# Kernel tuning notes

Hardware: AMD Instinct MI355X
Metric: run time of the kernel (lower is better)

## Reference

```python
import jax, jax.numpy as jnp
import numpy as np

L_RTN = 3  # complex taps produced by the RTN head (w_rtn3 out dim = 2*L_RTN)
EPS = 1e-12


def _to_complex(x):
    # (B, 2n) real interleaved [re0, im0, re1, im1, ...] -> (B, n) complex
    return x[:, 0::2] + 1j * x[:, 1::2]


def _to_real(xc):
    # (B, n) complex -> (B, 2n) real interleaved
    b, n = xc.shape
    return jnp.stack([xc.real, xc.imag], axis=-1).reshape(b, 2 * n)


def _complex_conv_taps(h_c, x_c):
    # per-sample causal complex FIR: out[t] = sum_l h[l] * x[t-l]
    # h_c: (B, L) complex, x_c: (B, n) complex
    n = x_c.shape[1]
    out = jnp.zeros_like(x_c)
    for l in range(h_c.shape[1]):  # L is tiny and static
        shifted = jnp.pad(x_c, ((0, 0), (l, 0)))[:, :n]
        out = out + h_c[:, l:l + 1] * shifted
    return out


def setup_inputs() -> dict:
    key = jax.random.key(0)
    ks = jax.random.split(key, 16)
    B, D_IN, H1, CH, H_RTN, H2, D_OUT = 8192, 512, 4096, 256, 1024, 4096, 512
    s = 0.02  # weight init scale
    x = jax.random.normal(ks[0], (B, D_IN), jnp.float32)
    w1 = s * jax.random.normal(ks[1], (H1, D_IN), jnp.float32)
    b1 = jnp.zeros((H1,), jnp.float32)
    w2 = s * jax.random.normal(ks[2], (CH, H1), jnp.float32)
    b2 = jnp.zeros((CH,), jnp.float32)
    w_rtn1 = s * jax.random.normal(ks[3], (H_RTN, CH), jnp.float32)
    b_rtn1 = jnp.zeros((H_RTN,), jnp.float32)
    w_rtn2 = s * jax.random.normal(ks[4], (H_RTN, H_RTN), jnp.float32)
    b_rtn2 = jnp.zeros((H_RTN,), jnp.float32)
    w_rtn3 = s * jax.random.normal(ks[5], (2 * L_RTN, H_RTN), jnp.float32)
    # bias so that RTN starts near identity tap [1, 0, 0, ...]
    b_rtn3 = jnp.zeros((2 * L_RTN,), jnp.float32).at[0].set(1.0)
    w3 = s * jax.random.normal(ks[6], (H2, CH), jnp.float32)
    b3 = jnp.zeros((H2,), jnp.float32)
    w4 = s * jax.random.normal(ks[7], (D_OUT, H2), jnp.float32)
    b4 = jnp.zeros((D_OUT,), jnp.float32)
    h = jax.random.normal(ks[8], (2,), jnp.float32)
    h = h / jnp.linalg.norm(h)  # unit-power single-tap fading channel
    noise = 0.1 * jax.random.normal(ks[9], (B, CH), jnp.float32)
    return {"x": x, "w1": w1, "b1": b1, "w2": w2, "b2": b2,
            "w_rtn1": w_rtn1, "b_rtn1": b_rtn1, "w_rtn2": w_rtn2,
            "b_rtn2": b_rtn2, "w_rtn3": w_rtn3, "b_rtn3": b_rtn3,
            "w3": w3, "b3": b3, "w4": w4, "b4": b4, "h": h, "noise": noise}


def reference(x, w1, b1, w2, b2, w_rtn1, b_rtn1, w_rtn2, b_rtn2,
              w_rtn3, b_rtn3, w3, b3, w4, b4, h, noise):
    # encoder (linear1 -> relu -> linear2)
    a = jax.nn.relu(x @ w1.T + b1)
    s = a @ w2.T + b2                      # (B, 2n) channel signal
    # power normalization: sqrt(2n) * sqrt(0.5) * s / ||s||
    scale = jnp.sqrt(s.shape[1] * 0.5)
    s = scale * s / jnp.linalg.norm(s, axis=1, keepdims=True)
    tx_c = _to_complex(s)                  # (B, n) transmitted symbols
    # single-tap complex channel
    h_c = h[0] + 1j * h[1]
    y = _to_real(h_c * tx_c) + noise       # add per-sample AWGN
    y_c = _to_complex(y)
    # LS channel estimate (1 tap): h_est = <y, x> / <x, x>
    num = jnp.sum(y_c * jnp.conj(tx_c), axis=1, keepdims=True)
    den = jnp.sum(jnp.abs(tx_c) ** 2, axis=1, keepdims=True)
    h_est = num / den                      # (B, 1)
    # zero-forcing signal estimate
    x_eq = y_c * jnp.conj(h_est) / (jnp.abs(h_est) ** 2 + EPS)
    xr = _to_real(x_eq)                    # (B, 2n)
    # RTN: predict inverse taps and apply per-sample complex conv
    g = jnp.tanh(xr @ w_rtn1.T + b_rtn1)
    g = jnp.tanh(g @ w_rtn2.T + b_rtn2)
    h_inv = g @ w_rtn3.T + b_rtn3          # (B, 2*L_RTN)
    h_inv_c = h_inv[:, 0::2] + 1j * h_inv[:, 1::2]
    xr = _to_real(_complex_conv_taps(h_inv_c, _to_complex(xr)))
    # decoder (linear3 -> relu -> linear4)
    out = jax.nn.relu(xr @ w3.T + b3)
    return out @ w4.T + b4
```

## Files before the change

### kernel.cpp

```cpp
#include <hip/hip_runtime.h>
#include <hip/hip_bf16.h>
#include <math.h>

using bf16 = __hip_bfloat16;
typedef __attribute__((ext_vector_type(8))) short short8;
typedef __attribute__((ext_vector_type(4))) float float4v;

template <typename T> __device__ inline T cvt_out(float v);
template <> __device__ inline float cvt_out<float>(float v) { return v; }
template <> __device__ inline bf16 cvt_out<bf16>(float v) { return __float2bfloat16(v); }

__device__ inline void gload_lds16(const bf16* g, bf16* l) {
    __builtin_amdgcn_global_load_lds(
        (const __attribute__((address_space(1))) void*)g,
        (__attribute__((address_space(3))) void*)l, 16, 0, 0);
}

struct CvtPack {
    const float* src[7];
    bf16* dst[7];
    int end[7];
};

__global__ __launch_bounds__(256) void cvt_all(CvtPack p) {
    int e = (blockIdx.x * 256 + threadIdx.x) * 4;
    int start = 0;
#pragma unroll
    for (int s = 0; s < 7; ++s) {
        if (e < p.end[s]) {
            int off = e - start;
            float4 v = *(const float4*)(p.src[s] + off);
            bf16* d = p.dst[s] + off;
            d[0] = __float2bfloat16(v.x);
            d[1] = __float2bfloat16(v.y);
            d[2] = __float2bfloat16(v.z);
            d[3] = __float2bfloat16(v.w);
            return;
        }
        start = p.end[s];
    }
}

__global__ __launch_bounds__(256) void reduce2_bias(const float* __restrict__ p0,
                                                    const float* __restrict__ p1,
                                                    const float* __restrict__ bias,
                                                    float* __restrict__ out,
                                                    int nmask, int total4) {
    int i = blockIdx.x * 256 + threadIdx.x;
    if (i < total4) {
        int idx = i * 4;
        float4 a = *(const float4*)(p0 + idx);
        float4 b = *(const float4*)(p1 + idx);
        float4 bb = *(const float4*)(bias + (idx & nmask));
        float4 r;
        r.x = a.x + b.x + bb.x;
        r.y = a.y + b.y + bb.y;
        r.z = a.z + b.z + bb.z;
        r.w = a.w + b.w + bb.w;
        *(float4*)(out + idx) = r;
    }
}

template <int ACT, typename OutT, int WMT, int WNT, int BKT, bool PARTIAL>
__global__ __launch_bounds__(256) void gemm_bt(const bf16* __restrict__ A,
                                               const bf16* __restrict__ W,
                                               const float* __restrict__ bias,
                                               OutT* __restrict__ C,
                                               int M, int N, int K,
                                               int nbn, int kcount) {
    constexpr int TBM = 32 * WMT;
    constexpr int TBN = 32 * WNT;
    constexpr int CPR = BKT / 8;
    constexpr int CA = TBM * CPR;
    constexpr int CB = TBN * CPR;

    __shared__ bf16 As[TBM * BKT];
    __shared__ bf16 Bs[TBN * BKT];

    const int bi = blockIdx.x;
    const int xcd = bi & 7, t = bi >> 3;
    const int bn = t % nbn;
    const int bm = xcd + 8 * (t / nbn);
    const int kbeg = PARTIAL ? blockIdx.y * kcount : 0;
    OutT* Cp = PARTIAL ? C + (size_t)blockIdx.y * M * N : C;

    const int tid = threadIdx.x;
    const int wave = tid >> 6, lane = tid & 63;
    const int wm = (wave >> 1) * (16 * WMT), wn = (wave & 1) * (16 * WNT);
    const int quad = lane >> 4, lrow = lane & 15;

    float4v acc[WMT][WNT] = {};
    const size_t arow = (size_t)(bm * TBM) * K;
    const size_t brow = (size_t)(bn * TBN) * K;

    for (int k0 = kbeg; k0 < kbeg + kcount; k0 += BKT) {
        __syncthreads();
#pragma unroll
        for (int tt = 0; tt < CA / 256; ++tt) {
            int base = tt * 256 + wave * 64;
            int c = base + lane;
            int row = c / CPR, col = (c % CPR) * 8;
            gload_lds16(A + arow + (size_t)row * K + k0 + col, As + base * 8);
        }
#pragma unroll
        for (int tt = 0; tt < CB / 256; ++tt) {
            int base = tt * 256 + wave * 64;
            int c = base + lane;
            int row = c / CPR, col = (c % CPR) * 8;
            gload_lds16(W + brow + (size_t)row * K + k0 + col, Bs + base * 8);
        }
        __syncthreads();
#pragma unroll
        for (int kk = 0; kk < BKT; kk += 32) {
            short8 af[WMT], bfr[WNT];
#pragma unroll
            for (int i = 0; i < WMT; ++i)
                af[i] = *(const short8*)(As + (wm + i * 16 + lrow) * BKT + kk + quad * 8);
#pragma unroll
            for (int j = 0; j < WNT; ++j)
                bfr[j] = *(const short8*)(Bs + (wn + j * 16 + lrow) * BKT + kk + quad * 8);
#pragma unroll
            for (int i = 0; i < WMT; ++i)
#pragma unroll
                for (int j = 0; j < WNT; ++j)
                    acc[i][j] = __builtin_amdgcn_mfma_f32_16x16x32_bf16(af[i], bfr[j], acc[i][j], 0, 0, 0);
        }
    }

#pragma unroll
    for (int i = 0; i < WMT; ++i) {
        int m0 = bm * TBM + wm + i * 16 + quad * 4;
#pragma unroll
        for (int j = 0; j < WNT; ++j) {
            int n = bn * TBN + wn + j * 16 + lrow;
            if constexpr (PARTIAL) {
#pragma unroll
                for (int r = 0; r < 4; ++r)
                    Cp[(size_t)(m0 + r) * N + n] = acc[i][j][r];
            } else {
                float bv = bias[n];
#pragma unroll
                for (int r = 0; r < 4; ++r) {
                    float v = acc[i][j][r] + bv;
                    if (ACT == 1) v = fmaxf(v, 0.f);
                    else if (ACT == 2) v = tanhf(v);
                    Cp[(size_t)(m0 + r) * N + n] = cvt_out<OutT>(v);
                }
            }
        }
    }
}

__global__ __launch_bounds__(64) void channel_kernel(const float* __restrict__ s,
                                                     const float* __restrict__ h,
                                                     const float* __restrict__ noise,
                                                     float* __restrict__ xr_f,
                                                     bf16* __restrict__ xr_b) {
    const int b = blockIdx.x, lane = threadIdx.x;
    const float* srow = s + (size_t)b * 256;

    float ss = 0.f;
#pragma unroll
    for (int t = 0; t < 4; ++t) {
        float v = srow[lane + 64 * t];
        ss += v * v;
    }
#pragma unroll
    for (int off = 32; off; off >>= 1) ss += __shfl_xor(ss, off);
    const float inv = sqrtf(128.0f) / sqrtf(ss);

    const float hre = h[0], him = h[1];

    float yre[2], yim[2];
    float nre = 0.f, nim = 0.f, den = 0.f;
#pragma unroll
    for (int t = 0; t < 2; ++t) {
        int c = lane + 64 * t;
        float tr = srow[2 * c] * inv, ti = srow[2 * c + 1] * inv;
        float yr = hre * tr - him * ti + noise[(size_t)b * 256 + 2 * c];
        float yi = hre * ti + him * tr + noise[(size_t)b * 256 + 2 * c + 1];
        yre[t] = yr; yim[t] = yi;
        nre += yr * tr + yi * ti;
        nim += yi * tr - yr * ti;
        den += tr * tr + ti * ti;
    }
#pragma unroll
    for (int off = 32; off; off >>= 1) {
        nre += __shfl_xor(nre, off);
        nim += __shfl_xor(nim, off);
        den += __shfl_xor(den, off);
    }
    const float her = nre / den, hei = nim / den;
    const float d2 = her * her + hei * hei + 1e-12f;

#pragma unroll
    for (int t = 0; t < 2; ++t) {
        int c = lane + 64 * t;
        float xre = (yre[t] * her + yim[t] * hei) / d2;
        float xim = (yim[t] * her - yre[t] * hei) / d2;
        xr_f[(size_t)b * 256 + 2 * c] = xre;
        xr_f[(size_t)b * 256 + 2 * c + 1] = xim;
        xr_b[(size_t)b * 256 + 2 * c] = __float2bfloat16(xre);
        xr_b[(size_t)b * 256 + 2 * c + 1] = __float2bfloat16(xim);
    }
}

__global__ __launch_bounds__(64) void rtn_taps_conv(const bf16* __restrict__ g2,
                                                    const float* __restrict__ wr3,
                                                    const float* __restrict__ br3,
                                                    const float* __restrict__ xr_f,
                                                    bf16* __restrict__ xr2) {
    const int b = blockIdx.x, lane = threadIdx.x;
    const bf16* grow = g2 + (size_t)b * 1024;

    float acc[6] = {0.f, 0.f, 0.f, 0.f, 0.f, 0.f};
#pragma unroll
    for (int t = 0; t < 16; ++t) {
        int k = lane + 64 * t;
        float gv = __bfloat162float(grow[k]);
#pragma unroll
        for (int j = 0; j < 6; ++j) acc[j] += gv * wr3[j * 1024 + k];
    }
#pragma unroll
    for (int j = 0; j < 6; ++j)
#pragma unroll
        for (int off = 32; off; off >>= 1) acc[j] += __shfl_xor(acc[j], off);

    float tre[3], tim[3];
#pragma unroll
    for (int l = 0; l < 3; ++l) {
        tre[l] = acc[2 * l] + br3[2 * l];
        tim[l] = acc[2 * l + 1] + br3[2 * l + 1];
    }

    const float* xrow = xr_f + (size_t)b * 256;
#pragma unroll
    for (int t = 0; t < 2; ++t) {
        int c = lane + 64 * t;
        float ore = 0.f, oim = 0.f;
#pragma unroll
        for (int l = 0; l < 3; ++l) {
            int cc = c - l;
            if (cc >= 0) {
                float xre = xrow[2 * cc], xim = xrow[2 * cc + 1];
                ore += tre[l] * xre - tim[l] * xim;
                oim += tre[l] * xim + tim[l] * xre;
            }
        }
        xr2[(size_t)b * 256 + 2 * c] = __float2bfloat16(ore);
        xr2[(size_t)b * 256 + 2 * c + 1] = __float2bfloat16(oim);
    }
}

extern "C" void kernel_launch(void* const* d_in, const int* in_sizes, int n_in,
                              void* d_out, int out_size, void* d_ws, size_t ws_size,
                              hipStream_t stream) {
    constexpr int B = 8192, D_IN = 512, H1 = 4096, CH = 256, HR = 1024, H2 = 4096, DOUT = 512;

    const float* x   = (const float*)d_in[0];
    const float* w1  = (const float*)d_in[1];
    const float* b1  = (const float*)d_in[2];
    const float* w2  = (const float*)d_in[3];
    const float* b2  = (const float*)d_in[4];
    const float* wr1 = (const float*)d_in[5];
    const float* br1 = (const float*)d_in[6];
    const float* wr2 = (const float*)d_in[7];
    const float* br2 = (const float*)d_in[8];
    const float* wr3 = (const float*)d_in[9];
    const float* br3 = (const float*)d_in[10];
    const float* w3  = (const float*)d_in[11];
    const float* b3  = (const float*)d_in[12];
    const float* w4  = (const float*)d_in[13];
    const float* b4  = (const float*)d_in[14];
    const float* h   = (const float*)d_in[15];
    const float* noise = (const float*)d_in[16];

    char* ws = (char*)d_ws;
    bf16*  a    = (bf16*)(ws + 0);
    bf16*  g1   = (bf16*)(ws + 0);
    bf16*  g2   = (bf16*)(ws + 16777216);
    bf16*  tbuf = (bf16*)(ws + 0);
    bf16*  xB   = (bf16*)(ws + 67108864);
    float* sF   = (float*)(ws + 75497472);
    float* xrF  = (float*)(ws + 83886080);
    bf16*  xrB  = (bf16*)(ws + 92274688);
    bf16*  xr2  = (bf16*)(ws + 96468992);
    bf16*  w1B  = (bf16*)(ws + 100663296);
    bf16*  w2B  = (bf16*)(ws + 104857600);
    bf16*  wr1B = (bf16*)(ws + 106954752);
    bf16*  wr2B = (bf16*)(ws + 107479040);
    bf16*  w3B  = (bf16*)(ws + 109576192);
    bf16*  w4B  = (bf16*)(ws + 111673344);

    float* g2P = (float*)(ws + 83886080);
    float* g6P = (float*)(ws + 67108864);

    dim3 blk(256);

    CvtPack p;
    const float* srcs[7] = {x, w1, w2, wr1, wr2, w3, w4};
    bf16* dsts[7] = {xB, w1B, w2B, wr1B, wr2B, w3B, w4B};
    int ns[7] = {B * D_IN, H1 * D_IN, CH * H1, HR * CH, HR * HR, H2 * CH, DOUT * H2};
    int cum = 0;
    for (int i = 0; i < 7; ++i) { p.src[i] = srcs[i]; p.dst[i] = dsts[i]; cum += ns[i]; p.end[i] = cum; }
    cvt_all<<<(cum / 4 + 255) / 256, blk, 0, stream>>>(p);

    gemm_bt<1, bf16, 4, 4, 64, false><<<64 * 32, blk, 0, stream>>>(
        xB, w1B, b1, a, B, H1, D_IN, 32, D_IN);
    gemm_bt<0, float, 2, 2, 128, true><<<dim3(128 * 4, 2), blk, 0, stream>>>(
        a, w2B, nullptr, g2P, B, CH, H1, 4, H1 / 2);
    reduce2_bias<<<(B * CH / 4 + 255) / 256, blk, 0, stream>>>(
        g2P, g2P + (size_t)B * CH, b2, sF, CH - 1, B * CH / 4);
    channel_kernel<<<B, 64, 0, stream>>>(sF, h, noise, xrF, xrB);
    gemm_bt<2, bf16, 4, 2, 64, false><<<64 * 16, blk, 0, stream>>>(
        xrB, wr1B, br1, g1, B, HR, CH, 16, CH);
    gemm_bt<2, bf16, 4, 2, 64, false><<<64 * 16, blk, 0, stream>>>(
        g1, wr2B, br2, g2, B, HR, HR, 16, HR);
    rtn_taps_conv<<<B, 64, 0, stream>>>(g2, wr3, br3, xrF, xr2);
    gemm_bt<1, bf16, 4, 4, 64, false><<<64 * 32, blk, 0, stream>>>(
        xr2, w3B, b3, tbuf, B, H2, CH, 32, CH);
    gemm_bt<0, float, 4, 2, 64, true><<<dim3(64 * 8, 2), blk, 0, stream>>>(
        tbuf, w4B, nullptr, g6P, B, DOUT, H2, 8, H2 / 2);
    reduce2_bias<<<(B * DOUT / 4 + 255) / 256, blk, 0, stream>>>(
        g6P, g6P + (size_t)B * DOUT, b4, (float*)d_out, DOUT - 1, B * DOUT / 4);
}
```

Measured before the change: 414.8 us.

## Stage GEMM epilogue through LDS for coalesced 16-byte stores, retune split-K

The GEMM epilogue now writes accumulator tiles into shared memory (reusing the staging buffer) and then stores them to global memory as coalesced 16-byte vectors, instead of scattered per-element stores. The w2 GEMM switches from a 2-way to a 4-way split-K with a different tile shape, and the partial-sum reduction becomes a templated K-way kernel. The workspace layout is rearranged to fit the larger partial buffer. This adds two barriers and extra shared-memory traffic per tile, in exchange for better store coalescing and more parallelism in the narrow GEMM.

```diff
diff --git a/kernel.cpp b/kernel.cpp
--- a/kernel.cpp
+++ b/kernel.cpp
@@ -41,22 +41,21 @@
     }
 }
 
-__global__ __launch_bounds__(256) void reduce2_bias(const float* __restrict__ p0,
-                                                    const float* __restrict__ p1,
+template <int NK>
+__global__ __launch_bounds__(256) void reduceK_bias(const float* __restrict__ p,
                                                     const float* __restrict__ bias,
                                                     float* __restrict__ out,
-                                                    int nmask, int total4) {
+                                                    size_t mn, int nmask, int total4) {
     int i = blockIdx.x * 256 + threadIdx.x;
     if (i < total4) {
         int idx = i * 4;
-        float4 a = *(const float4*)(p0 + idx);
-        float4 b = *(const float4*)(p1 + idx);
         float4 bb = *(const float4*)(bias + (idx & nmask));
-        float4 r;
-        r.x = a.x + b.x + bb.x;
-        r.y = a.y + b.y + bb.y;
-        r.z = a.z + b.z + bb.z;
-        r.w = a.w + b.w + bb.w;
+        float4 r = bb;
+#pragma unroll
+        for (int k = 0; k < NK; ++k) {
+            float4 a = *(const float4*)(p + k * mn + idx);
+            r.x += a.x; r.y += a.y; r.z += a.z; r.w += a.w;
+        }
         *(float4*)(out + idx) = r;
     }
 }
@@ -73,9 +72,13 @@
     constexpr int CPR = BKT / 8;
     constexpr int CA = TBM * CPR;
     constexpr int CB = TBN * CPR;
-
-    __shared__ bf16 As[TBM * BKT];
-    __shared__ bf16 Bs[TBN * BKT];
+    constexpr int STAGE_B = (TBM + TBN) * BKT * 2;
+    constexpr int REPACK_B = TBM * TBN * (int)sizeof(OutT);
+    constexpr int SH = STAGE_B > REPACK_B ? STAGE_B : REPACK_B;
+
+    __shared__ __align__(16) char smem[SH];
+    bf16* As = (bf16*)smem;
+    bf16* Bs = As + TBM * BKT;
 
     const int bi = blockIdx.x;
     const int xcd = bi & 7, t = bi >> 3;
@@ -127,27 +130,37 @@
         }
     }
 
+    __syncthreads();
+    OutT* R = (OutT*)smem;
 #pragma unroll
     for (int i = 0; i < WMT; ++i) {
-        int m0 = bm * TBM + wm + i * 16 + quad * 4;
+        int row0 = wm + i * 16 + quad * 4;
 #pragma unroll
         for (int j = 0; j < WNT; ++j) {
-            int n = bn * TBN + wn + j * 16 + lrow;
-            if constexpr (PARTIAL) {
-#pragma unroll
-                for (int r = 0; r < 4; ++r)
-                    Cp[(size_t)(m0 + r) * N + n] = acc[i][j][r];
-            } else {
-                float bv = bias[n];
-#pragma unroll
-                for (int r = 0; r < 4; ++r) {
-                    float v = acc[i][j][r] + bv;
+            int col = wn + j * 16 + lrow;
+            float bv = 0.f;
+            if constexpr (!PARTIAL) bv = bias[bn * TBN + col];
+#pragma unroll
+            for (int r = 0; r < 4; ++r) {
+                float v = acc[i][j][r] + bv;
+                if constexpr (!PARTIAL) {
                     if (ACT == 1) v = fmaxf(v, 0.f);
                     else if (ACT == 2) v = tanhf(v);
-                    Cp[(size_t)(m0 + r) * N + n] = cvt_out<OutT>(v);
                 }
+                R[(row0 + r) * TBN + col] = cvt_out<OutT>(v);
             }
         }
+    }
+    __syncthreads();
+    constexpr int EPC = 16 / (int)sizeof(OutT);
+    constexpr int CR = TBN / EPC;
+    constexpr int TOT = TBM * CR;
+#pragma unroll
+    for (int t2 = 0; t2 < TOT / 256; ++t2) {
+        int c = t2 * 256 + tid;
+        int row = c / CR, cin = c % CR;
+        float4 v = *((const float4*)smem + c);
+        *(float4*)&Cp[(size_t)(bm * TBM + row) * N + bn * TBN + cin * EPC] = v;
     }
 }
 
@@ -280,20 +293,20 @@
     bf16*  g1   = (bf16*)(ws + 0);
     bf16*  g2   = (bf16*)(ws + 16777216);
     bf16*  tbuf = (bf16*)(ws + 0);
-    bf16*  xB   = (bf16*)(ws + 67108864);
-    float* sF   = (float*)(ws + 75497472);
-    float* xrF  = (float*)(ws + 83886080);
-    bf16*  xrB  = (bf16*)(ws + 92274688);
-    bf16*  xr2  = (bf16*)(ws + 96468992);
-    bf16*  w1B  = (bf16*)(ws + 100663296);
-    bf16*  w2B  = (bf16*)(ws + 104857600);
-    bf16*  wr1B = (bf16*)(ws + 106954752);
-    bf16*  wr2B = (bf16*)(ws + 107479040);
-    bf16*  w3B  = (bf16*)(ws + 109576192);
-    bf16*  w4B  = (bf16*)(ws + 111673344);
-
-    float* g2P = (float*)(ws + 83886080);
-    float* g6P = (float*)(ws + 67108864);
+    bf16*  w1B  = (bf16*)(ws + 67108864);
+    bf16*  w2B  = (bf16*)(ws + 71303168);
+    bf16*  wr1B = (bf16*)(ws + 73400320);
+    bf16*  wr2B = (bf16*)(ws + 73924608);
+    bf16*  w3B  = (bf16*)(ws + 76021760);
+    bf16*  w4B  = (bf16*)(ws + 78118912);
+    bf16*  xB   = (bf16*)(ws + 82313216);
+    float* sF   = (float*)(ws + 90701824);
+    float* xrF  = (float*)(ws + 99090432);
+    bf16*  xrB  = (bf16*)(ws + 107479040);
+    bf16*  xr2  = (bf16*)(ws + 111673344);
+
+    float* g2P = (float*)(ws + 82313216);
+    float* g6P = (float*)(ws + 82313216);
 
     dim3 blk(256);
 
@@ -307,10 +320,10 @@
 
     gemm_bt<1, bf16, 4, 4, 64, false><<<64 * 32, blk, 0, stream>>>(
         xB, w1B, b1, a, B, H1, D_IN, 32, D_IN);
-    gemm_bt<0, float, 2, 2, 128, true><<<dim3(128 * 4, 2), blk, 0, stream>>>(
-        a, w2B, nullptr, g2P, B, CH, H1, 4, H1 / 2);
-    reduce2_bias<<<(B * CH / 4 + 255) / 256, blk, 0, stream>>>(
-        g2P, g2P + (size_t)B * CH, b2, sF, CH - 1, B * CH / 4);
+    gemm_bt<0, float, 4, 2, 64, true><<<dim3(64 * 4, 4), blk, 0, stream>>>(
+        a, w2B, nullptr, g2P, B, CH, H1, 4, H1 / 4);
+    reduceK_bias<4><<<(B * CH / 4 + 255) / 256, blk, 0, stream>>>(
+        g2P, b2, sF, (size_t)B * CH, CH - 1, B * CH / 4);
     channel_kernel<<<B, 64, 0, stream>>>(sF, h, noise, xrF, xrB);
     gemm_bt<2, bf16, 4, 2, 64, false><<<64 * 16, blk, 0, stream>>>(
         xrB, wr1B, br1, g1, B, HR, CH, 16, CH);
@@ -321,6 +334,6 @@
         xr2, w3B, b3, tbuf, B, H2, CH, 32, CH);
     gemm_bt<0, float, 4, 2, 64, true><<<dim3(64 * 8, 2), blk, 0, stream>>>(
         tbuf, w4B, nullptr, g6P, B, DOUT, H2, 8, H2 / 2);
-    reduce2_bias<<<(B * DOUT / 4 + 255) / 256, blk, 0, stream>>>(
-        g6P, g6P + (size_t)B * DOUT, b4, (float*)d_out, DOUT - 1, B * DOUT / 4);
-}
+    reduceK_bias<2><<<(B * DOUT / 4 + 255) / 256, blk, 0, stream>>>(
+        g6P, b4, (float*)d_out, (size_t)B * DOUT, DOUT - 1, B * DOUT / 4);
+}
```

Result: faster. 387.9 us (-6.5%).
